# Kernel optimization log

Measured on AMD Instinct MI355X. Metric: run time of the kernel, lower is better.

Reference implementation:

```python
import jax, jax.numpy as jnp
import numpy as np

T, B = 1024, 256
OBS, ACT, GOAL = 64, 8, 16
NH, NH2 = 64, 64
H = NH + NH2  # 128 LSTM hidden


def _lin_init(k, out_d, in_d):
    bound = 1.0 / np.sqrt(in_d)
    k1, k2 = jax.random.split(k)
    w = jax.random.uniform(k1, (out_d, in_d), minval=-bound, maxval=bound, dtype=jnp.float32)
    b = jax.random.uniform(k2, (out_d,), minval=-bound, maxval=bound, dtype=jnp.float32)
    return w, b


def setup_inputs() -> dict:
    key = jax.random.key(0)
    ks = jax.random.split(key, 18)
    inp = {
        'observations': jax.random.normal(ks[0], (T, B, OBS), dtype=jnp.float32),
        'lps': jax.random.normal(ks[1], (T, B, 1), dtype=jnp.float32),
        'goal_eps': jax.random.normal(ks[2], (T, B, GOAL), dtype=jnp.float32),
        'action_eps': jax.random.normal(ks[3], (T, B, ACT), dtype=jnp.float32),
        'h0': jnp.zeros((2, B, H), jnp.float32),
        'c0': jnp.zeros((2, B, H), jnp.float32),
    }
    # LSTM (2 layers), torch layout: w_ih [4H, in], w_hh [4H, H]
    inp['w_ih0'], inp['b_ih0'] = _lin_init(ks[4], 4 * H, OBS + 1)
    inp['w_hh0'], inp['b_hh0'] = _lin_init(ks[5], 4 * H, H)
    inp['w_ih1'], inp['b_ih1'] = _lin_init(ks[6], 4 * H, H)
    inp['w_hh1'], inp['b_hh1'] = _lin_init(ks[7], 4 * H, H)
    # goal_decoder: MLP(NH, 2*GOAL), hidden = max(64, 32) = 64
    inp['gd_w1'], inp['gd_b1'] = _lin_init(ks[8], 64, NH)
    inp['gd_w2'], inp['gd_b2'] = _lin_init(ks[9], 2 * GOAL, 64)
    # action_decoder: MLP(GOAL+OBS=80, 2*ACT), hidden = 80
    inp['ad_w1'], inp['ad_b1'] = _lin_init(ks[10], GOAL + OBS, GOAL + OBS)
    inp['ad_w2'], inp['ad_b2'] = _lin_init(ks[11], 2 * ACT, GOAL + OBS)
    # value_decoder: MLP(80, 1), hidden = 80
    inp['vd_w1'], inp['vd_b1'] = _lin_init(ks[12], GOAL + OBS, GOAL + OBS)
    inp['vd_w2'], inp['vd_b2'] = _lin_init(ks[13], 1, GOAL + OBS)
    # lp_decoder: MLP(H+OBS=192, 1), hidden = 192
    inp['lpd_w1'], inp['lpd_b1'] = _lin_init(ks[14], H + OBS, H + OBS)
    inp['lpd_w2'], inp['lpd_b2'] = _lin_init(ks[15], 1, H + OBS)
    return inp


def _lstm_layer(x, h, c, wi, wh, bi, bh):
    def step(carry, xt):
        h, c = carry
        g = xt @ wi.T + h @ wh.T + (bi + bh)
        i, f, gg, o = jnp.split(g, 4, axis=-1)  # torch gate order: i, f, g, o
        i, f, o = jax.nn.sigmoid(i), jax.nn.sigmoid(f), jax.nn.sigmoid(o)
        c = f * c + i * jnp.tanh(gg)
        h = o * jnp.tanh(c)
        return (h, c), h
    _, hs = jax.lax.scan(step, (h, c), x)
    return hs  # [T, B, H]


def _mlp(x, w1, b1, w2, b2):
    return jax.nn.relu(x @ w1.T + b1) @ w2.T + b2


def _diag_logprob(x, mu, var):
    # log N(x; mu, diag(var))
    d = x.shape[-1]
    LOG_2PI = jnp.float32(np.log(2.0 * np.pi))
    return -0.5 * (jnp.sum((x - mu) ** 2 / var + jnp.log(var), axis=-1) + d * LOG_2PI)


def reference(observations, lps, goal_eps, action_eps, h0, c0,
              w_ih0, b_ih0, w_hh0, b_hh0, w_ih1, b_ih1, w_hh1, b_hh1,
              gd_w1, gd_b1, gd_w2, gd_b2, ad_w1, ad_b1, ad_w2, ad_b2,
              vd_w1, vd_b1, vd_w2, vd_b2, lpd_w1, lpd_b1, lpd_w2, lpd_b2):
    x = jnp.concatenate([observations, lps], axis=2)  # [T, B, OBS+1]
    h1 = _lstm_layer(x, h0[0], c0[0], w_ih0, w_hh0, b_ih0, b_hh0)
    latents_full = _lstm_layer(h1, h0[1], c0[1], w_ih1, w_hh1, b_ih1, b_hh1)  # [T,B,H]
    full_lat_obs = jnp.concatenate([latents_full, observations], axis=2)
    latents = latents_full[:, :, :NH]

    gm, gs = jnp.split(_mlp(latents, gd_w1, gd_b1, gd_w2, gd_b2), 2, axis=2)
    gm = 100.0 * jnp.tanh(gm * 0.001)
    gs = jnp.tanh(gs)
    gvar = gs ** 2 + 0.001
    goals = jax.lax.stop_gradient(gm + jnp.sqrt(gvar) * goal_eps)  # .sample() is non-diff
    log_prob_goals = _diag_logprob(goals, gm, gvar)

    goal_obs = jnp.concatenate([goals, observations], axis=2)
    am, asd = jnp.split(_mlp(goal_obs, ad_w1, ad_b1, ad_w2, ad_b2), 2, axis=2)
    avar = asd ** 2 + 0.001
    actions = jax.lax.stop_gradient(am + jnp.sqrt(avar) * action_eps)
    log_prob_actions = _diag_logprob(actions, am, avar)

    values = _mlp(goal_obs, vd_w1, vd_b1, vd_w2, vd_b2)
    lp_values = _mlp(full_lat_obs, lpd_w1, lpd_b1, lpd_w2, lpd_b2)
    return (actions, log_prob_actions, goals, log_prob_goals, values, lp_values)
```

## Files before the change

### kernel.cpp

```cpp
#include <hip/hip_runtime.h>
#include <hip/hip_bf16.h>
#include <math.h>

#define TT 1024
#define BB 256
#define LOG2PI 1.8378770664093453f

typedef short short8 __attribute__((ext_vector_type(8)));
typedef float f32x4  __attribute__((ext_vector_type(4)));

__device__ __forceinline__ float sigmoid_f(float x) {
    return 1.f / (1.f + __expf(-x));
}
__device__ __forceinline__ float tanh_f(float x) {
    return 1.f - 2.f / (__expf(2.f*x) + 1.f);
}
__device__ __forceinline__ unsigned short f2bf(float x) {
    unsigned int u = __float_as_uint(x);
    unsigned int r = (u + 0x7FFFu + ((u >> 16) & 1u)) >> 16;
    return (unsigned short)r;
}

#define MF(acc, a, bfr) acc = __builtin_amdgcn_mfma_f32_16x16x32_bf16((a), (bfr), (acc), 0, 0, 0)

__global__ __launch_bounds__(256) void cvt_bf16_kernel(
    const float* __restrict__ in, unsigned short* __restrict__ out)
{
    const int i = blockIdx.x*256 + threadIdx.x;
    const float4 a = ((const float4*)in)[2*i];
    const float4 b = ((const float4*)in)[2*i + 1];
    short8 v;
    v[0]=(short)f2bf(a.x); v[1]=(short)f2bf(a.y);
    v[2]=(short)f2bf(a.z); v[3]=(short)f2bf(a.w);
    v[4]=(short)f2bf(b.x); v[5]=(short)f2bf(b.y);
    v[6]=(short)f2bf(b.z); v[7]=(short)f2bf(b.w);
    ((short8*)out)[i] = v;
}

__global__ __launch_bounds__(256) void init_state_kernel(
    const float* __restrict__ h0, const float* __restrict__ c0,
    float* __restrict__ h_state, float* __restrict__ c_state)
{
    const int idx = blockIdx.x*256 + threadIdx.x;
    h_state[idx] = h0[idx];
    c_state[idx] = c0[idx];
}

__global__ __launch_bounds__(512, 2) void lstm0_kernel(
    const unsigned short* __restrict__ xb,
    const float* __restrict__ lps,
    const float* __restrict__ wi0,
    const float* __restrict__ wh0,
    const float* __restrict__ bi0, const float* __restrict__ bh0,
    float* __restrict__ h_state, float* __restrict__ c_state,
    unsigned short* __restrict__ h1_all,
    int steps)
{
    const int tid  = threadIdx.x;
    const int wave = tid >> 6;
    const int lane = tid & 63;
    const int b    = blockIdx.x;
    const int col  = lane & 15;
    const int kg   = lane >> 4;
    const int m    = wave*16 + col;

    __shared__ __align__(16) unsigned short s1_bf[2][128];

    short8 whf[4][4];
    short8 wxf[4][2];
    f32x4 wc64, bias4;
    #pragma unroll
    for (int tn = 0; tn < 4; ++tn) {
        const int j = tn*128 + m;
        #pragma unroll
        for (int ks = 0; ks < 4; ++ks) {
            const float* s = wh0 + (size_t)j*128 + ks*32 + kg*8;
            short8 v;
            #pragma unroll
            for (int i = 0; i < 8; ++i) v[i] = (short)f2bf(s[i]);
            whf[tn][ks] = v;
        }
        #pragma unroll
        for (int ks = 0; ks < 2; ++ks) {
            const float* s = wi0 + (size_t)j*65 + ks*32 + kg*8;
            short8 v;
            #pragma unroll
            for (int i = 0; i < 8; ++i) v[i] = (short)f2bf(s[i]);
            wxf[tn][ks] = v;
        }
        wc64[tn]  = wi0[(size_t)j*65 + 64];
        bias4[tn] = bi0[j] + bh0[j];
    }

    float c1 = 0.f, s1l = 0.f;
    if (kg == 0) {
        s1l = h_state[b*128 + m];
        c1  = c_state[b*128 + m];
        s1_bf[0][m] = f2bf(s1l);
    }
    const unsigned short* xp = xb + (size_t)b*64 + kg*8;
    const float* lpp = lps + b;
    short8 xA0 = *(const short8*)(xp);
    short8 xA1 = *(const short8*)(xp + 32);
    float  lpA = *lpp;
    xp  += (size_t)BB*64;
    lpp += BB;
    unsigned short* h1p = h1_all + (size_t)b*128 + m;

    asm volatile("s_waitcnt lgkmcnt(0)" ::: "memory");
    __builtin_amdgcn_s_barrier();
    __builtin_amdgcn_sched_barrier(0);

    #define STEP0(T_, RB, WB)                                                   \
    {                                                                           \
        short8 af0 = *(const short8*)&s1_bf[RB][0*32 + kg*8];                   \
        short8 af1 = *(const short8*)&s1_bf[RB][1*32 + kg*8];                   \
        short8 af2 = *(const short8*)&s1_bf[RB][2*32 + kg*8];                   \
        short8 af3 = *(const short8*)&s1_bf[RB][3*32 + kg*8];                   \
        short8 xu0 = xA0, xu1 = xA1;  float lpu = lpA;       \
        if ((T_) + 1 < steps) {                                                 \
            xA0 = *(const short8*)(xp);                                         \
            xA1 = *(const short8*)(xp + 32);                                    \
            lpA = *lpp;                                                         \
        }                                                                       \
        xp += (size_t)BB*64;  lpp += BB;                                        \
        f32x4 a0 = {0.f,0.f,0.f,0.f}, a1 = a0, a2 = a0, a3 = a0;                \
        MF(a0, af0, whf[0][0]); MF(a1, af0, whf[1][0]);                         \
        MF(a2, af0, whf[2][0]); MF(a3, af0, whf[3][0]);                         \
        MF(a0, af1, whf[0][1]); MF(a1, af1, whf[1][1]);                         \
        MF(a2, af1, whf[2][1]); MF(a3, af1, whf[3][1]);                         \
        MF(a0, af2, whf[0][2]); MF(a1, af2, whf[1][2]);                         \
        MF(a2, af2, whf[2][2]); MF(a3, af2, whf[3][2]);                         \
        MF(a0, af3, whf[0][3]); MF(a1, af3, whf[1][3]);                         \
        MF(a2, af3, whf[2][3]); MF(a3, af3, whf[3][3]);                         \
        MF(a0, xu0, wxf[0][0]); MF(a1, xu0, wxf[1][0]);                         \
        MF(a2, xu0, wxf[2][0]); MF(a3, xu0, wxf[3][0]);                         \
        MF(a0, xu1, wxf[0][1]); MF(a1, xu1, wxf[1][1]);                         \
        MF(a2, xu1, wxf[2][1]); MF(a3, xu1, wxf[3][1]);                         \
        if (kg == 0) {                                                          \
            float gi = a0[0] + bias4[0] + wc64[0]*lpu;                          \
            float gf = a1[0] + bias4[1] + wc64[1]*lpu;                          \
            float gg = a2[0] + bias4[2] + wc64[2]*lpu;                          \
            float go = a3[0] + bias4[3] + wc64[3]*lpu;                          \
            float iv = sigmoid_f(gi);                                           \
            float fv = sigmoid_f(gf);                                           \
            float gv = tanh_f(gg);                                              \
            float ov = sigmoid_f(go);                                           \
            c1 = fmaf(fv, c1, iv*gv);                                           \
            float hv = ov * tanh_f(c1);                                         \
            s1l = hv;                                                           \
            unsigned short hb = f2bf(hv);                                       \
            s1_bf[WB][m] = hb;                                                  \
            *h1p = hb;                                                          \
        }                                                                       \
        h1p += (size_t)BB*128;                                                  \
        asm volatile("s_waitcnt lgkmcnt(0)" ::: "memory");                      \
        __builtin_amdgcn_s_barrier();                                           \
        __builtin_amdgcn_sched_barrier(0);                                      \
    }

    for (int t = 0; t < steps; t += 2) {
        STEP0(t,     0, 1);
        STEP0(t + 1, 1, 0);
    }
    #undef STEP0

    if (kg == 0) {
        h_state[b*128 + m] = s1l;
        c_state[b*128 + m] = c1;
    }
}

__global__ __launch_bounds__(512, 2) void lstm1_kernel(
    const unsigned short* __restrict__ h1_all,
    const float* __restrict__ wi1, const float* __restrict__ wh1,
    const float* __restrict__ bi1, const float* __restrict__ bh1,
    float* __restrict__ h_state, float* __restrict__ c_state,
    float* __restrict__ h2_all,
    int steps)
{
    const int tid  = threadIdx.x;
    const int wave = tid >> 6;
    const int lane = tid & 63;
    const int b    = blockIdx.x;
    const int col  = lane & 15;
    const int kg   = lane >> 4;
    const int m    = wave*16 + col;

    __shared__ __align__(16) unsigned short s2_bf[2][128];

    short8 wif[4][4], whf[4][4];
    f32x4 bias4;
    #pragma unroll
    for (int tn = 0; tn < 4; ++tn) {
        const int j = tn*128 + m;
        #pragma unroll
        for (int ks = 0; ks < 4; ++ks) {
            const int ko = ks*32 + kg*8;
            const float* sa = wi1 + (size_t)j*128 + ko;
            const float* sb = wh1 + (size_t)j*128 + ko;
            short8 va, vb;
            #pragma unroll
            for (int i = 0; i < 8; ++i) {
                va[i] = (short)f2bf(sa[i]);
                vb[i] = (short)f2bf(sb[i]);
            }
            wif[tn][ks] = va;  whf[tn][ks] = vb;
        }
        bias4[tn] = bi1[j] + bh1[j];
    }

    float c2 = 0.f, s2l = 0.f;
    if (kg == 0) {
        s2l = h_state[b*128 + m];
        c2  = c_state[b*128 + m];
        s2_bf[0][m] = f2bf(s2l);
    }
    const unsigned short* sp = h1_all + (size_t)b*128 + kg*8;
    short8 sA0 = *(const short8*)(sp);
    short8 sA1 = *(const short8*)(sp + 32);
    short8 sA2 = *(const short8*)(sp + 64);
    short8 sA3 = *(const short8*)(sp + 96);
    sp += (size_t)BB*128;
    float* h2p = h2_all + (size_t)b*128 + m;

    asm volatile("s_waitcnt lgkmcnt(0)" ::: "memory");
    __builtin_amdgcn_s_barrier();
    __builtin_amdgcn_sched_barrier(0);

    #define STEP1(T_, RB, WB)                                                   \
    {                                                                           \
        short8 xu0 = sA0, xu1 = sA1, xu2 = sA2, xu3 = sA3;         \
        if ((T_) + 1 < steps) {                                                 \
            sA0 = *(const short8*)(sp);                                         \
            sA1 = *(const short8*)(sp + 32);                                    \
            sA2 = *(const short8*)(sp + 64);                                    \
            sA3 = *(const short8*)(sp + 96);                                    \
        }                                                                       \
        sp += (size_t)BB*128;                                                   \
        short8 af0 = *(const short8*)&s2_bf[RB][0*32 + kg*8];                   \
        short8 af1 = *(const short8*)&s2_bf[RB][1*32 + kg*8];                   \
        short8 af2 = *(const short8*)&s2_bf[RB][2*32 + kg*8];                   \
        short8 af3 = *(const short8*)&s2_bf[RB][3*32 + kg*8];                   \
        f32x4 b0 = {0.f,0.f,0.f,0.f}, b1 = b0, b2 = b0, b3 = b0;                \
        MF(b0, xu0, wif[0][0]); MF(b1, xu0, wif[1][0]);                         \
        MF(b2, xu0, wif[2][0]); MF(b3, xu0, wif[3][0]);                         \
        MF(b0, xu1, wif[0][1]); MF(b1, xu1, wif[1][1]);                         \
        MF(b2, xu1, wif[2][1]); MF(b3, xu1, wif[3][1]);                         \
        MF(b0, xu2, wif[0][2]); MF(b1, xu2, wif[1][2]);                         \
        MF(b2, xu2, wif[2][2]); MF(b3, xu2, wif[3][2]);                         \
        MF(b0, xu3, wif[0][3]); MF(b1, xu3, wif[1][3]);                         \
        MF(b2, xu3, wif[2][3]); MF(b3, xu3, wif[3][3]);                         \
        MF(b0, af0, whf[0][0]); MF(b1, af0, whf[1][0]);                         \
        MF(b2, af0, whf[2][0]); MF(b3, af0, whf[3][0]);                         \
        MF(b0, af1, whf[0][1]); MF(b1, af1, whf[1][1]);                         \
        MF(b2, af1, whf[2][1]); MF(b3, af1, whf[3][1]);                         \
        MF(b0, af2, whf[0][2]); MF(b1, af2, whf[1][2]);                         \
        MF(b2, af2, whf[2][2]); MF(b3, af2, whf[3][2]);                         \
        MF(b0, af3, whf[0][3]); MF(b1, af3, whf[1][3]);                         \
        MF(b2, af3, whf[2][3]); MF(b3, af3, whf[3][3]);                         \
        if (kg == 0) {                                                          \
            float iv = sigmoid_f(b0[0] + bias4[0]);                             \
            float fv = sigmoid_f(b1[0] + bias4[1]);                             \
            float gv = tanh_f   (b2[0] + bias4[2]);                             \
            float ov = sigmoid_f(b3[0] + bias4[3]);                             \
            c2 = fmaf(fv, c2, iv*gv);                                           \
            float hv = ov * tanh_f(c2);                                         \
            s2l = hv;                                                           \
            s2_bf[WB][m] = f2bf(hv);                                            \
            *h2p = hv;                                                          \
        }                                                                       \
        h2p += (size_t)BB*128;                                                  \
        asm volatile("s_waitcnt lgkmcnt(0)" ::: "memory");                      \
        __builtin_amdgcn_s_barrier();                                           \
        __builtin_amdgcn_sched_barrier(0);                                      \
    }

    for (int t = 0; t < steps; t += 2) {
        STEP1(t,     0, 1);
        STEP1(t + 1, 1, 0);
    }
    #undef STEP1

    if (kg == 0) {
        h_state[b*128 + m] = s2l;
        c_state[b*128 + m] = c2;
    }
}

__global__ __launch_bounds__(256) void dec_goal_kernel(
    const float* __restrict__ h2,
    const float* __restrict__ geps,
    const float* __restrict__ w1, const float* __restrict__ b1,
    const float* __restrict__ w2, const float* __restrict__ b2,
    float* __restrict__ out_goals, float* __restrict__ out_lpg)
{
    __shared__ float W1[64*64];
    __shared__ float W2[32*64];
    __shared__ float B1[64];
    __shared__ float B2[32];
    const int tid = threadIdx.x;
    for (int e = tid; e < 64*64; e += 256) W1[e] = w1[e];
    for (int e = tid; e < 32*64; e += 256) W2[e] = w2[e];
    if (tid < 64) B1[tid] = b1[tid];
    if (tid < 32) B2[tid] = b2[tid];
    __syncthreads();

    const size_t row = (size_t)blockIdx.x*256 + tid;
    const float* xr = h2 + row*128;

    float hid[64];
    #pragma unroll
    for (int jj = 0; jj < 64; ++jj) hid[jj] = B1[jj];
    for (int k = 0; k < 64; k += 4) {
        float4 xv = *(const float4*)(xr + k);
        #pragma unroll
        for (int jj = 0; jj < 64; ++jj) {
            float s = hid[jj];
            s = fmaf(W1[jj*64 + k],     xv.x, s);
            s = fmaf(W1[jj*64 + k + 1], xv.y, s);
            s = fmaf(W1[jj*64 + k + 2], xv.z, s);
            s = fmaf(W1[jj*64 + k + 3], xv.w, s);
            hid[jj] = s;
        }
    }
    #pragma unroll
    for (int jj = 0; jj < 64; ++jj) hid[jj] = fmaxf(hid[jj], 0.f);

    float gm[16];
    #pragma unroll
    for (int jj = 0; jj < 16; ++jj) {
        float s = B2[jj];
        #pragma unroll
        for (int k = 0; k < 64; ++k) s = fmaf(W2[jj*64 + k], hid[k], s);
        gm[jj] = 100.f * tanh_f(0.001f * s);
    }
    float ge[16];
    #pragma unroll
    for (int d = 0; d < 16; d += 4) {
        float4 v = *(const float4*)(geps + row*16 + d);
        ge[d]=v.x; ge[d+1]=v.y; ge[d+2]=v.z; ge[d+3]=v.w;
    }
    float lsum = 0.f;
    float goalv[16];
    #pragma unroll
    for (int jj = 0; jj < 16; ++jj) {
        float s = B2[16 + jj];
        #pragma unroll
        for (int k = 0; k < 64; ++k) s = fmaf(W2[(16+jj)*64 + k], hid[k], s);
        float gs   = tanh_f(s);
        float gvar = fmaf(gs, gs, 0.001f);
        float goal = fmaf(sqrtf(gvar), ge[jj], gm[jj]);
        goalv[jj] = goal;
        float dd = goal - gm[jj];
        lsum += dd*dd/gvar + __logf(gvar);
    }
    #pragma unroll
    for (int d = 0; d < 16; d += 4) {
        float4 v = make_float4(goalv[d], goalv[d+1], goalv[d+2], goalv[d+3]);
        *(float4*)(out_goals + row*16 + d) = v;
    }
    out_lpg[row] = -0.5f*(lsum + 16.f*LOG2PI);
}

__global__ __launch_bounds__(256) void dec_av_kernel(
    const float* __restrict__ goals,
    const float* __restrict__ obs,
    const float* __restrict__ aeps,
    const float* __restrict__ aw1, const float* __restrict__ ab1,
    const float* __restrict__ aw2, const float* __restrict__ ab2,
    const float* __restrict__ vw1, const float* __restrict__ vb1,
    const float* __restrict__ vw2, const float* __restrict__ vb2,
    float* __restrict__ out_actions, float* __restrict__ out_lpa,
    float* __restrict__ out_values)
{
    __shared__ float AW1[80*80];
    __shared__ float VW1[80*80];
    __shared__ float AW2[16*80];
    __shared__ float VW2[80];
    __shared__ float AB1[80];
    __shared__ float VB1[80];
    __shared__ float AB2[16];
    const int tid = threadIdx.x;
    for (int e = tid; e < 80*80; e += 256) { AW1[e] = aw1[e]; VW1[e] = vw1[e]; }
    for (int e = tid; e < 16*80; e += 256) AW2[e] = aw2[e];
    if (tid < 80) { VW2[tid] = vw2[tid]; AB1[tid] = ab1[tid]; VB1[tid] = vb1[tid]; }
    if (tid < 16) AB2[tid] = ab2[tid];
    __syncthreads();

    const size_t row = (size_t)blockIdx.x*256 + tid;

    float hid[80];
    #pragma unroll
    for (int jj = 0; jj < 80; ++jj) hid[jj] = AB1[jj];
    for (int k = 0; k < 80; k += 4) {
        float4 xv;
        if (k < 16) xv = *(const float4*)(goals + row*16 + k);
        else        xv = *(const float4*)(obs + row*64 + (k - 16));
        #pragma unroll
        for (int jj = 0; jj < 80; ++jj) {
            float s = hid[jj];
            s = fmaf(AW1[jj*80 + k],     xv.x, s);
            s = fmaf(AW1[jj*80 + k + 1], xv.y, s);
            s = fmaf(AW1[jj*80 + k + 2], xv.z, s);
            s = fmaf(AW1[jj*80 + k + 3], xv.w, s);
            hid[jj] = s;
        }
    }
    #pragma unroll
    for (int jj = 0; jj < 80; ++jj) hid[jj] = fmaxf(hid[jj], 0.f);

    float am[8], asd[8];
    #pragma unroll
    for (int jj = 0; jj < 8; ++jj) {
        float s = AB2[jj];
        #pragma unroll
        for (int k = 0; k < 80; ++k) s = fmaf(AW2[jj*80 + k], hid[k], s);
        am[jj] = s;
    }
    #pragma unroll
    for (int jj = 0; jj < 8; ++jj) {
        float s = AB2[8 + jj];
        #pragma unroll
        for (int k = 0; k < 80; ++k) s = fmaf(AW2[(8+jj)*80 + k], hid[k], s);
        asd[jj] = s;
    }

    float ae[8];
    #pragma unroll
    for (int d = 0; d < 8; d += 4) {
        float4 v = *(const float4*)(aeps + row*8 + d);
        ae[d]=v.x; ae[d+1]=v.y; ae[d+2]=v.z; ae[d+3]=v.w;
    }
    float lsum = 0.f;
    float actv[8];
    #pragma unroll
    for (int d = 0; d < 8; ++d) {
        float avar = fmaf(asd[d], asd[d], 0.001f);
        float act  = fmaf(sqrtf(avar), ae[d], am[d]);
        actv[d] = act;
        float dd = act - am[d];
        lsum += dd*dd/avar + __logf(avar);
    }
    #pragma unroll
    for (int d = 0; d < 8; d += 4) {
        float4 v = make_float4(actv[d], actv[d+1], actv[d+2], actv[d+3]);
        *(float4*)(out_actions + row*8 + d) = v;
    }
    out_lpa[row] = -0.5f*(lsum + 8.f*LOG2PI);

    float vh[80];
    #pragma unroll
    for (int jj = 0; jj < 80; ++jj) vh[jj] = VB1[jj];
    for (int k = 0; k < 80; k += 4) {
        float4 xv;
        if (k < 16) xv = *(const float4*)(goals + row*16 + k);
        else        xv = *(const float4*)(obs + row*64 + (k - 16));
        #pragma unroll
        for (int jj = 0; jj < 80; ++jj) {
            float s = vh[jj];
            s = fmaf(VW1[jj*80 + k],     xv.x, s);
            s = fmaf(VW1[jj*80 + k + 1], xv.y, s);
            s = fmaf(VW1[jj*80 + k + 2], xv.z, s);
            s = fmaf(VW1[jj*80 + k + 3], xv.w, s);
            vh[jj] = s;
        }
    }
    float v = vb2[0];
    #pragma unroll
    for (int jj = 0; jj < 80; ++jj) v = fmaf(VW2[jj], fmaxf(vh[jj], 0.f), v);
    out_values[row] = v;
}

__global__ __launch_bounds__(256) void dec_lpv_kernel(
    const float* __restrict__ h2,
    const float* __restrict__ obs,
    const float* __restrict__ w1, const float* __restrict__ b1,
    const float* __restrict__ w2, const float* __restrict__ b2,
    float* __restrict__ out_lpv)
{
    __shared__ __align__(16) float W1s[64*192];
    __shared__ float B1[192];
    __shared__ float W2[192];
    const int tid = threadIdx.x;
    const int l = tid & 3;
    const size_t item = (size_t)blockIdx.x*64 + (tid >> 2);
    if (tid < 192) { B1[tid] = b1[tid]; W2[tid] = w2[tid]; }

    float x[48];
    #pragma unroll
    for (int q = 0; q < 12; ++q) {
        int gk = l*48 + q*4;
        float4 v;
        if (gk < 128) v = *(const float4*)(h2 + item*128 + gk);
        else          v = *(const float4*)(obs + item*64 + (gk - 128));
        x[q*4]=v.x; x[q*4+1]=v.y; x[q*4+2]=v.z; x[q*4+3]=v.w;
    }

    float acc = 0.f;
    for (int j0 = 0; j0 < 192; j0 += 64) {
        __syncthreads();
        for (int e = tid; e < 64*48; e += 256) {
            int rr = e / 48, q = e - rr*48;
            *(float4*)&W1s[rr*192 + q*4] =
                *(const float4*)&w1[(size_t)(j0 + rr)*192 + q*4];
        }
        __syncthreads();
        for (int jj = 0; jj < 64; ++jj) {
            const float* wr = W1s + jj*192 + l*48;
            float p = 0.f;
            #pragma unroll
            for (int q = 0; q < 12; ++q) {
                float4 wv = *(const float4*)(wr + q*4);
                p = fmaf(wv.x, x[q*4],     p);
                p = fmaf(wv.y, x[q*4 + 1], p);
                p = fmaf(wv.z, x[q*4 + 2], p);
                p = fmaf(wv.w, x[q*4 + 3], p);
            }
            p += __shfl_xor(p, 1);
            p += __shfl_xor(p, 2);
            float h = fmaxf(p + B1[j0 + jj], 0.f);
            acc = fmaf(W2[j0 + jj], h, acc);
        }
    }
    if (l == 0) out_lpv[item] = acc + b2[0];
}

extern "C" void kernel_launch(void* const* d_in, const int* in_sizes, int n_in,
                              void* d_out, int out_size, void* d_ws, size_t ws_size,
                              hipStream_t stream)
{
    (void)in_sizes; (void)n_in; (void)out_size;

    const float* obs    = (const float*)d_in[0];
    const float* lps    = (const float*)d_in[1];
    const float* geps   = (const float*)d_in[2];
    const float* aeps   = (const float*)d_in[3];
    const float* h0     = (const float*)d_in[4];
    const float* c0     = (const float*)d_in[5];
    const float* w_ih0  = (const float*)d_in[6];
    const float* b_ih0  = (const float*)d_in[7];
    const float* w_hh0  = (const float*)d_in[8];
    const float* b_hh0  = (const float*)d_in[9];
    const float* w_ih1  = (const float*)d_in[10];
    const float* b_ih1  = (const float*)d_in[11];
    const float* w_hh1  = (const float*)d_in[12];
    const float* b_hh1  = (const float*)d_in[13];
    const float* gd_w1  = (const float*)d_in[14];
    const float* gd_b1  = (const float*)d_in[15];
    const float* gd_w2  = (const float*)d_in[16];
    const float* gd_b2  = (const float*)d_in[17];
    const float* ad_w1  = (const float*)d_in[18];
    const float* ad_b1  = (const float*)d_in[19];
    const float* ad_w2  = (const float*)d_in[20];
    const float* ad_b2  = (const float*)d_in[21];
    const float* vd_w1  = (const float*)d_in[22];
    const float* vd_b1  = (const float*)d_in[23];
    const float* vd_w2  = (const float*)d_in[24];
    const float* vd_b2  = (const float*)d_in[25];
    const float* lpd_w1 = (const float*)d_in[26];
    const float* lpd_b1 = (const float*)d_in[27];
    const float* lpd_w2 = (const float*)d_in[28];
    const float* lpd_b2 = (const float*)d_in[29];

    float* out         = (float*)d_out;
    float* out_actions = out;
    float* out_lpa     = out + 2097152;
    float* out_goals   = out + 2359296;
    float* out_lpg     = out + 6553600;
    float* out_values  = out + 6815744;
    float* out_lpv     = out + 7077888;

    const size_t XB_ELEMS    = (size_t)TT * BB * 64;
    const size_t STATE_ELEMS = 2ull * BB * 128;
    int C = 0;
    for (int c = TT; c >= 8; c >>= 1) {
        size_t need = XB_ELEMS*2
                    + (size_t)c * BB * 128 * 2
                    + (size_t)c * BB * 128 * 4
                    + 2 * STATE_ELEMS * 4;
        if (need <= ws_size) { C = c; break; }
    }
    if (C == 0) return;
    const int nchunks = TT / C;

    unsigned short* xb  = (unsigned short*)d_ws;
    unsigned short* h1c = xb + XB_ELEMS;
    float* h2c     = (float*)(h1c + (size_t)C * BB * 128);
    float* h_state = h2c + (size_t)C * BB * 128;
    float* c_state = h_state + STATE_ELEMS;

    const dim3 blk(256);

    cvt_bf16_kernel<<<dim3((int)(XB_ELEMS/8/256)), blk, 0, stream>>>(obs, xb);
    init_state_kernel<<<dim3((int)(STATE_ELEMS/256)), blk, 0, stream>>>(
        h0, c0, h_state, c_state);

    for (int ch = 0; ch < nchunks; ++ch) {
        const size_t crow0 = (size_t)ch * C * BB;
        const int rows = C * BB;

        lstm0_kernel<<<dim3(BB), dim3(512), 0, stream>>>(
            xb + crow0*64, lps + crow0, w_ih0, w_hh0, b_ih0, b_hh0,
            h_state, c_state, h1c, C);

        lstm1_kernel<<<dim3(BB), dim3(512), 0, stream>>>(
            h1c, w_ih1, w_hh1, b_ih1, b_hh1,
            h_state + BB*128, c_state + BB*128, h2c, C);

        dec_goal_kernel<<<dim3(rows/256), blk, 0, stream>>>(
            h2c, geps + crow0*16, gd_w1, gd_b1, gd_w2, gd_b2,
            out_goals + crow0*16, out_lpg + crow0);

        dec_av_kernel<<<dim3(rows/256), blk, 0, stream>>>(
            out_goals + crow0*16, obs + crow0*64, aeps + crow0*8,
            ad_w1, ad_b1, ad_w2, ad_b2, vd_w1, vd_b1, vd_w2, vd_b2,
            out_actions + crow0*8, out_lpa + crow0, out_values + crow0);

        dec_lpv_kernel<<<dim3(rows/64), blk, 0, stream>>>(
            h2c, obs + crow0*64, lpd_w1, lpd_b1, lpd_w2, lpd_b2,
            out_lpv + crow0);
    }
}
```

Before: 2.377 ms.

## Precompute next step's input-projection MFMAs before the barrier in LSTM kernels

Moves the input-to-hidden MFMA work for step t+1 to the end of step t, after the gate update and before the barrier, so the critical path after each barrier holds only the recurrent h@Wh MFMAs. Global loads of x/h1 now run two steps ahead. Launch bounds drop from 2 to 1 blocks per CU, giving the compiler more registers for the live accumulators. This cuts serial latency per timestep but may lower occupancy.

Result: slower. 2.669 ms (+12.3%).

```diff
diff --git a/kernel.cpp b/kernel.cpp
--- a/kernel.cpp
+++ b/kernel.cpp
@@ -46,7 +46,7 @@
     c_state[idx] = c0[idx];
 }
 
-__global__ __launch_bounds__(512, 2) void lstm0_kernel(
+__global__ __launch_bounds__(512, 1) void lstm0_kernel(
     const unsigned short* __restrict__ xb,
     const float* __restrict__ lps,
     const float* __restrict__ wi0,
@@ -102,9 +102,21 @@
     const float* lpp = lps + b;
     short8 xA0 = *(const short8*)(xp);
     short8 xA1 = *(const short8*)(xp + 32);
-    float  lpA = *lpp;
-    xp  += (size_t)BB*64;
+    xp += (size_t)BB*64;
+    float lpA = *lpp;
     lpp += BB;
+
+    f32x4 a0 = {0.f,0.f,0.f,0.f}, a1 = a0, a2 = a0, a3 = a0;
+    MF(a0, xA0, wxf[0][0]); MF(a1, xA0, wxf[1][0]);
+    MF(a2, xA0, wxf[2][0]); MF(a3, xA0, wxf[3][0]);
+    MF(a0, xA1, wxf[0][1]); MF(a1, xA1, wxf[1][1]);
+    MF(a2, xA1, wxf[2][1]); MF(a3, xA1, wxf[3][1]);
+    if (steps > 1) {
+        xA0 = *(const short8*)(xp);
+        xA1 = *(const short8*)(xp + 32);
+    }
+    xp += (size_t)BB*64;
+
     unsigned short* h1p = h1_all + (size_t)b*128 + m;
 
     asm volatile("s_waitcnt lgkmcnt(0)" ::: "memory");
@@ -117,14 +129,6 @@
         short8 af1 = *(const short8*)&s1_bf[RB][1*32 + kg*8];                   \
         short8 af2 = *(const short8*)&s1_bf[RB][2*32 + kg*8];                   \
         short8 af3 = *(const short8*)&s1_bf[RB][3*32 + kg*8];                   \
-        short8 xu0 = xA0, xu1 = xA1;  float lpu = lpA;       \
-        if ((T_) + 1 < steps) {                                                 \
-            xA0 = *(const short8*)(xp);                                         \
-            xA1 = *(const short8*)(xp + 32);                                    \
-            lpA = *lpp;                                                         \
-        }                                                                       \
-        xp += (size_t)BB*64;  lpp += BB;                                        \
-        f32x4 a0 = {0.f,0.f,0.f,0.f}, a1 = a0, a2 = a0, a3 = a0;                \
         MF(a0, af0, whf[0][0]); MF(a1, af0, whf[1][0]);                         \
         MF(a2, af0, whf[2][0]); MF(a3, af0, whf[3][0]);                         \
         MF(a0, af1, whf[0][1]); MF(a1, af1, whf[1][1]);                         \
@@ -133,15 +137,11 @@
         MF(a2, af2, whf[2][2]); MF(a3, af2, whf[3][2]);                         \
         MF(a0, af3, whf[0][3]); MF(a1, af3, whf[1][3]);                         \
         MF(a2, af3, whf[2][3]); MF(a3, af3, whf[3][3]);                         \
-        MF(a0, xu0, wxf[0][0]); MF(a1, xu0, wxf[1][0]);                         \
-        MF(a2, xu0, wxf[2][0]); MF(a3, xu0, wxf[3][0]);                         \
-        MF(a0, xu1, wxf[0][1]); MF(a1, xu1, wxf[1][1]);                         \
-        MF(a2, xu1, wxf[2][1]); MF(a3, xu1, wxf[3][1]);                         \
         if (kg == 0) {                                                          \
-            float gi = a0[0] + bias4[0] + wc64[0]*lpu;                          \
-            float gf = a1[0] + bias4[1] + wc64[1]*lpu;                          \
-            float gg = a2[0] + bias4[2] + wc64[2]*lpu;                          \
-            float go = a3[0] + bias4[3] + wc64[3]*lpu;                          \
+            float gi = a0[0] + bias4[0] + wc64[0]*lpA;                          \
+            float gf = a1[0] + bias4[1] + wc64[1]*lpA;                          \
+            float gg = a2[0] + bias4[2] + wc64[2]*lpA;                          \
+            float go = a3[0] + bias4[3] + wc64[3]*lpA;                          \
             float iv = sigmoid_f(gi);                                           \
             float fv = sigmoid_f(gf);                                           \
             float gv = tanh_f(gg);                                              \
@@ -154,6 +154,18 @@
             *h1p = hb;                                                          \
         }                                                                       \
         h1p += (size_t)BB*128;                                                  \
+        if ((T_) + 1 < steps) lpA = *lpp;     \
+        lpp += BB;                                                              \
+        a0 = (f32x4){0.f,0.f,0.f,0.f}; a1 = a0; a2 = a0; a3 = a0;               \
+        MF(a0, xA0, wxf[0][0]); MF(a1, xA0, wxf[1][0]);                         \
+        MF(a2, xA0, wxf[2][0]); MF(a3, xA0, wxf[3][0]);                         \
+        MF(a0, xA1, wxf[0][1]); MF(a1, xA1, wxf[1][1]);                         \
+        MF(a2, xA1, wxf[2][1]); MF(a3, xA1, wxf[3][1]);                         \
+        if ((T_) + 2 < steps) {                 \
+            xA0 = *(const short8*)(xp);                                         \
+            xA1 = *(const short8*)(xp + 32);                                    \
+        }                                                                       \
+        xp += (size_t)BB*64;                                                    \
         asm volatile("s_waitcnt lgkmcnt(0)" ::: "memory");                      \
         __builtin_amdgcn_s_barrier();                                           \
         __builtin_amdgcn_sched_barrier(0);                                      \
@@ -171,7 +183,7 @@
     }
 }
 
-__global__ __launch_bounds__(512, 2) void lstm1_kernel(
+__global__ __launch_bounds__(512, 1) void lstm1_kernel(
     const unsigned short* __restrict__ h1_all,
     const float* __restrict__ wi1, const float* __restrict__ wh1,
     const float* __restrict__ bi1, const float* __restrict__ bh1,
@@ -222,6 +234,24 @@
     short8 sA2 = *(const short8*)(sp + 64);
     short8 sA3 = *(const short8*)(sp + 96);
     sp += (size_t)BB*128;
+
+    f32x4 b0 = {0.f,0.f,0.f,0.f}, b1 = b0, b2 = b0, b3 = b0;
+    MF(b0, sA0, wif[0][0]); MF(b1, sA0, wif[1][0]);
+    MF(b2, sA0, wif[2][0]); MF(b3, sA0, wif[3][0]);
+    MF(b0, sA1, wif[0][1]); MF(b1, sA1, wif[1][1]);
+    MF(b2, sA1, wif[2][1]); MF(b3, sA1, wif[3][1]);
+    MF(b0, sA2, wif[0][2]); MF(b1, sA2, wif[1][2]);
+    MF(b2, sA2, wif[2][2]); MF(b3, sA2, wif[3][2]);
+    MF(b0, sA3, wif[0][3]); MF(b1, sA3, wif[1][3]);
+    MF(b2, sA3, wif[2][3]); MF(b3, sA3, wif[3][3]);
+    if (steps > 1) {
+        sA0 = *(const short8*)(sp);
+        sA1 = *(const short8*)(sp + 32);
+        sA2 = *(const short8*)(sp + 64);
+        sA3 = *(const short8*)(sp + 96);
+    }
+    sp += (size_t)BB*128;
+
     float* h2p = h2_all + (size_t)b*128 + m;
 
     asm volatile("s_waitcnt lgkmcnt(0)" ::: "memory");
@@ -230,27 +260,10 @@
 
     #define STEP1(T_, RB, WB)                                                   \
     {                                                                           \
-        short8 xu0 = sA0, xu1 = sA1, xu2 = sA2, xu3 = sA3;         \
-        if ((T_) + 1 < steps) {                                                 \
-            sA0 = *(const short8*)(sp);                                         \
-            sA1 = *(const short8*)(sp + 32);                                    \
-            sA2 = *(const short8*)(sp + 64);                                    \
-            sA3 = *(const short8*)(sp + 96);                                    \
-        }                                                                       \
-        sp += (size_t)BB*128;                                                   \
         short8 af0 = *(const short8*)&s2_bf[RB][0*32 + kg*8];                   \
         short8 af1 = *(const short8*)&s2_bf[RB][1*32 + kg*8];                   \
         short8 af2 = *(const short8*)&s2_bf[RB][2*32 + kg*8];                   \
         short8 af3 = *(const short8*)&s2_bf[RB][3*32 + kg*8];                   \
-        f32x4 b0 = {0.f,0.f,0.f,0.f}, b1 = b0, b2 = b0, b3 = b0;                \
-        MF(b0, xu0, wif[0][0]); MF(b1, xu0, wif[1][0]);                         \
-        MF(b2, xu0, wif[2][0]); MF(b3, xu0, wif[3][0]);                         \
-        MF(b0, xu1, wif[0][1]); MF(b1, xu1, wif[1][1]);                         \
-        MF(b2, xu1, wif[2][1]); MF(b3, xu1, wif[3][1]);                         \
-        MF(b0, xu2, wif[0][2]); MF(b1, xu2, wif[1][2]);                         \
-        MF(b2, xu2, wif[2][2]); MF(b3, xu2, wif[3][2]);                         \
-        MF(b0, xu3, wif[0][3]); MF(b1, xu3, wif[1][3]);                         \
-        MF(b2, xu3, wif[2][3]); MF(b3, xu3, wif[3][3]);                         \
         MF(b0, af0, whf[0][0]); MF(b1, af0, whf[1][0]);                         \
         MF(b2, af0, whf[2][0]); MF(b3, af0, whf[3][0]);                         \
         MF(b0, af1, whf[0][1]); MF(b1, af1, whf[1][1]);                         \
@@ -271,6 +284,22 @@
             *h2p = hv;                                                          \
         }                                                                       \
         h2p += (size_t)BB*128;                                                  \
+        b0 = (f32x4){0.f,0.f,0.f,0.f}; b1 = b0; b2 = b0; b3 = b0;               \
+        MF(b0, sA0, wif[0][0]); MF(b1, sA0, wif[1][0]);                         \
+        MF(b2, sA0, wif[2][0]); MF(b3, sA0, wif[3][0]);                         \
+        MF(b0, sA1, wif[0][1]); MF(b1, sA1, wif[1][1]);                         \
+        MF(b2, sA1, wif[2][1]); MF(b3, sA1, wif[3][1]);                         \
+        MF(b0, sA2, wif[0][2]); MF(b1, sA2, wif[1][2]);                         \
+        MF(b2, sA2, wif[2][2]); MF(b3, sA2, wif[3][2]);                         \
+        MF(b0, sA3, wif[0][3]); MF(b1, sA3, wif[1][3]);                         \
+        MF(b2, sA3, wif[2][3]); MF(b3, sA3, wif[3][3]);                         \
+        if ((T_) + 2 < steps) {                 \
+            sA0 = *(const short8*)(sp);                                         \
+            sA1 = *(const short8*)(sp + 32);                                    \
+            sA2 = *(const short8*)(sp + 64);                                    \
+            sA3 = *(const short8*)(sp + 96);                                    \
+        }                                                                       \
+        sp += (size_t)BB*128;                                                   \
         asm volatile("s_waitcnt lgkmcnt(0)" ::: "memory");                      \
         __builtin_amdgcn_s_barrier();                                           \
         __builtin_amdgcn_sched_barrier(0);                                      \
```

## Fuse both LSTM layers into one producer-consumer kernel with progress flags

Applied to the files above, without the earlier changes.

Replaces the two sequential LSTM kernels with one launch of 2*BB blocks. The first half runs layer 0 and publishes per-batch progress counters with release stores. The second half runs layer 1, spin-waiting on those counters every 8 steps, so the two recurrences overlap in time instead of running back to back. The gain depends on all 512 blocks being co-resident, since producers and consumers spin on each other. It also adds polling and acquire/release overhead plus a small reset kernel per chunk.

New measurement: 6.515 ms. 2.74x slower.

```diff
diff --git a/kernel.cpp b/kernel.cpp
--- a/kernel.cpp
+++ b/kernel.cpp
@@ -46,245 +46,283 @@
     c_state[idx] = c0[idx];
 }
 
-__global__ __launch_bounds__(512, 2) void lstm0_kernel(
+__global__ __launch_bounds__(256) void reset_prog_kernel(unsigned* prog)
+{
+    prog[threadIdx.x] = 0u;
+}
+
+__global__ __launch_bounds__(512, 2) void lstm_pc_kernel(
     const unsigned short* __restrict__ xb,
     const float* __restrict__ lps,
     const float* __restrict__ wi0,
     const float* __restrict__ wh0,
     const float* __restrict__ bi0, const float* __restrict__ bh0,
-    float* __restrict__ h_state, float* __restrict__ c_state,
-    unsigned short* __restrict__ h1_all,
-    int steps)
-{
-    const int tid  = threadIdx.x;
-    const int wave = tid >> 6;
-    const int lane = tid & 63;
-    const int b    = blockIdx.x;
-    const int col  = lane & 15;
-    const int kg   = lane >> 4;
-    const int m    = wave*16 + col;
-
-    __shared__ __align__(16) unsigned short s1_bf[2][128];
-
-    short8 whf[4][4];
-    short8 wxf[4][2];
-    f32x4 wc64, bias4;
-    #pragma unroll
-    for (int tn = 0; tn < 4; ++tn) {
-        const int j = tn*128 + m;
-        #pragma unroll
-        for (int ks = 0; ks < 4; ++ks) {
-            const float* s = wh0 + (size_t)j*128 + ks*32 + kg*8;
-            short8 v;
-            #pragma unroll
-            for (int i = 0; i < 8; ++i) v[i] = (short)f2bf(s[i]);
-            whf[tn][ks] = v;
-        }
-        #pragma unroll
-        for (int ks = 0; ks < 2; ++ks) {
-            const float* s = wi0 + (size_t)j*65 + ks*32 + kg*8;
-            short8 v;
-            #pragma unroll
-            for (int i = 0; i < 8; ++i) v[i] = (short)f2bf(s[i]);
-            wxf[tn][ks] = v;
-        }
-        wc64[tn]  = wi0[(size_t)j*65 + 64];
-        bias4[tn] = bi0[j] + bh0[j];
-    }
-
-    float c1 = 0.f, s1l = 0.f;
-    if (kg == 0) {
-        s1l = h_state[b*128 + m];
-        c1  = c_state[b*128 + m];
-        s1_bf[0][m] = f2bf(s1l);
-    }
-    const unsigned short* xp = xb + (size_t)b*64 + kg*8;
-    const float* lpp = lps + b;
-    short8 xA0 = *(const short8*)(xp);
-    short8 xA1 = *(const short8*)(xp + 32);
-    float  lpA = *lpp;
-    xp  += (size_t)BB*64;
-    lpp += BB;
-    unsigned short* h1p = h1_all + (size_t)b*128 + m;
-
-    asm volatile("s_waitcnt lgkmcnt(0)" ::: "memory");
-    __builtin_amdgcn_s_barrier();
-    __builtin_amdgcn_sched_barrier(0);
-
-    #define STEP0(T_, RB, WB)                                                   \
-    {                                                                           \
-        short8 af0 = *(const short8*)&s1_bf[RB][0*32 + kg*8];                   \
-        short8 af1 = *(const short8*)&s1_bf[RB][1*32 + kg*8];                   \
-        short8 af2 = *(const short8*)&s1_bf[RB][2*32 + kg*8];                   \
-        short8 af3 = *(const short8*)&s1_bf[RB][3*32 + kg*8];                   \
-        short8 xu0 = xA0, xu1 = xA1;  float lpu = lpA;       \
-        if ((T_) + 1 < steps) {                                                 \
-            xA0 = *(const short8*)(xp);                                         \
-            xA1 = *(const short8*)(xp + 32);                                    \
-            lpA = *lpp;                                                         \
-        }                                                                       \
-        xp += (size_t)BB*64;  lpp += BB;                                        \
-        f32x4 a0 = {0.f,0.f,0.f,0.f}, a1 = a0, a2 = a0, a3 = a0;                \
-        MF(a0, af0, whf[0][0]); MF(a1, af0, whf[1][0]);                         \
-        MF(a2, af0, whf[2][0]); MF(a3, af0, whf[3][0]);                         \
-        MF(a0, af1, whf[0][1]); MF(a1, af1, whf[1][1]);                         \
-        MF(a2, af1, whf[2][1]); MF(a3, af1, whf[3][1]);                         \
-        MF(a0, af2, whf[0][2]); MF(a1, af2, whf[1][2]);                         \
-        MF(a2, af2, whf[2][2]); MF(a3, af2, whf[3][2]);                         \
-        MF(a0, af3, whf[0][3]); MF(a1, af3, whf[1][3]);                         \
-        MF(a2, af3, whf[2][3]); MF(a3, af3, whf[3][3]);                         \
-        MF(a0, xu0, wxf[0][0]); MF(a1, xu0, wxf[1][0]);                         \
-        MF(a2, xu0, wxf[2][0]); MF(a3, xu0, wxf[3][0]);                         \
-        MF(a0, xu1, wxf[0][1]); MF(a1, xu1, wxf[1][1]);                         \
-        MF(a2, xu1, wxf[2][1]); MF(a3, xu1, wxf[3][1]);                         \
-        if (kg == 0) {                                                          \
-            float gi = a0[0] + bias4[0] + wc64[0]*lpu;                          \
-            float gf = a1[0] + bias4[1] + wc64[1]*lpu;                          \
-            float gg = a2[0] + bias4[2] + wc64[2]*lpu;                          \
-            float go = a3[0] + bias4[3] + wc64[3]*lpu;                          \
-            float iv = sigmoid_f(gi);                                           \
-            float fv = sigmoid_f(gf);                                           \
-            float gv = tanh_f(gg);                                              \
-            float ov = sigmoid_f(go);                                           \
-            c1 = fmaf(fv, c1, iv*gv);                                           \
-            float hv = ov * tanh_f(c1);                                         \
-            s1l = hv;                                                           \
-            unsigned short hb = f2bf(hv);                                       \
-            s1_bf[WB][m] = hb;                                                  \
-            *h1p = hb;                                                          \
-        }                                                                       \
-        h1p += (size_t)BB*128;                                                  \
-        asm volatile("s_waitcnt lgkmcnt(0)" ::: "memory");                      \
-        __builtin_amdgcn_s_barrier();                                           \
-        __builtin_amdgcn_sched_barrier(0);                                      \
-    }
-
-    for (int t = 0; t < steps; t += 2) {
-        STEP0(t,     0, 1);
-        STEP0(t + 1, 1, 0);
-    }
-    #undef STEP0
-
-    if (kg == 0) {
-        h_state[b*128 + m] = s1l;
-        c_state[b*128 + m] = c1;
-    }
-}
-
-__global__ __launch_bounds__(512, 2) void lstm1_kernel(
-    const unsigned short* __restrict__ h1_all,
+    unsigned short* h1_all,
     const float* __restrict__ wi1, const float* __restrict__ wh1,
     const float* __restrict__ bi1, const float* __restrict__ bh1,
     float* __restrict__ h_state, float* __restrict__ c_state,
     float* __restrict__ h2_all,
+    unsigned* prog,
     int steps)
 {
     const int tid  = threadIdx.x;
     const int wave = tid >> 6;
     const int lane = tid & 63;
-    const int b    = blockIdx.x;
     const int col  = lane & 15;
     const int kg   = lane >> 4;
     const int m    = wave*16 + col;
 
-    __shared__ __align__(16) unsigned short s2_bf[2][128];
-
-    short8 wif[4][4], whf[4][4];
-    f32x4 bias4;
-    #pragma unroll
-    for (int tn = 0; tn < 4; ++tn) {
-        const int j = tn*128 + m;
-        #pragma unroll
-        for (int ks = 0; ks < 4; ++ks) {
-            const int ko = ks*32 + kg*8;
-            const float* sa = wi1 + (size_t)j*128 + ko;
-            const float* sb = wh1 + (size_t)j*128 + ko;
-            short8 va, vb;
+    __shared__ __align__(16) unsigned short st_bf[2][128];
+
+    if (blockIdx.x < BB) {
+        const int b = blockIdx.x;
+        unsigned* pg = prog + b;
+
+        short8 whf[4][4];
+        short8 wxf[4][2];
+        f32x4 wc64, bias4;
+        #pragma unroll
+        for (int tn = 0; tn < 4; ++tn) {
+            const int j = tn*128 + m;
             #pragma unroll
-            for (int i = 0; i < 8; ++i) {
-                va[i] = (short)f2bf(sa[i]);
-                vb[i] = (short)f2bf(sb[i]);
+            for (int ks = 0; ks < 4; ++ks) {
+                const float* s = wh0 + (size_t)j*128 + ks*32 + kg*8;
+                short8 v;
+                #pragma unroll
+                for (int i = 0; i < 8; ++i) v[i] = (short)f2bf(s[i]);
+                whf[tn][ks] = v;
             }
-            wif[tn][ks] = va;  whf[tn][ks] = vb;
-        }
-        bias4[tn] = bi1[j] + bh1[j];
-    }
-
-    float c2 = 0.f, s2l = 0.f;
-    if (kg == 0) {
-        s2l = h_state[b*128 + m];
-        c2  = c_state[b*128 + m];
-        s2_bf[0][m] = f2bf(s2l);
-    }
-    const unsigned short* sp = h1_all + (size_t)b*128 + kg*8;
-    short8 sA0 = *(const short8*)(sp);
-    short8 sA1 = *(const short8*)(sp + 32);
-    short8 sA2 = *(const short8*)(sp + 64);
-    short8 sA3 = *(const short8*)(sp + 96);
-    sp += (size_t)BB*128;
-    float* h2p = h2_all + (size_t)b*128 + m;
-
-    asm volatile("s_waitcnt lgkmcnt(0)" ::: "memory");
-    __builtin_amdgcn_s_barrier();
-    __builtin_amdgcn_sched_barrier(0);
-
-    #define STEP1(T_, RB, WB)                                                   \
-    {                                                                           \
-        short8 xu0 = sA0, xu1 = sA1, xu2 = sA2, xu3 = sA3;         \
-        if ((T_) + 1 < steps) {                                                 \
-            sA0 = *(const short8*)(sp);                                         \
-            sA1 = *(const short8*)(sp + 32);                                    \
-            sA2 = *(const short8*)(sp + 64);                                    \
-            sA3 = *(const short8*)(sp + 96);                                    \
-        }                                                                       \
-        sp += (size_t)BB*128;                                                   \
-        short8 af0 = *(const short8*)&s2_bf[RB][0*32 + kg*8];                   \
-        short8 af1 = *(const short8*)&s2_bf[RB][1*32 + kg*8];                   \
-        short8 af2 = *(const short8*)&s2_bf[RB][2*32 + kg*8];                   \
-        short8 af3 = *(const short8*)&s2_bf[RB][3*32 + kg*8];                   \
-        f32x4 b0 = {0.f,0.f,0.f,0.f}, b1 = b0, b2 = b0, b3 = b0;                \
-        MF(b0, xu0, wif[0][0]); MF(b1, xu0, wif[1][0]);                         \
-        MF(b2, xu0, wif[2][0]); MF(b3, xu0, wif[3][0]);                         \
-        MF(b0, xu1, wif[0][1]); MF(b1, xu1, wif[1][1]);                         \
-        MF(b2, xu1, wif[2][1]); MF(b3, xu1, wif[3][1]);                         \
-        MF(b0, xu2, wif[0][2]); MF(b1, xu2, wif[1][2]);                         \
-        MF(b2, xu2, wif[2][2]); MF(b3, xu2, wif[3][2]);                         \
-        MF(b0, xu3, wif[0][3]); MF(b1, xu3, wif[1][3]);                         \
-        MF(b2, xu3, wif[2][3]); MF(b3, xu3, wif[3][3]);                         \
-        MF(b0, af0, whf[0][0]); MF(b1, af0, whf[1][0]);                         \
-        MF(b2, af0, whf[2][0]); MF(b3, af0, whf[3][0]);                         \
-        MF(b0, af1, whf[0][1]); MF(b1, af1, whf[1][1]);                         \
-        MF(b2, af1, whf[2][1]); MF(b3, af1, whf[3][1]);                         \
-        MF(b0, af2, whf[0][2]); MF(b1, af2, whf[1][2]);                         \
-        MF(b2, af2, whf[2][2]); MF(b3, af2, whf[3][2]);                         \
-        MF(b0, af3, whf[0][3]); MF(b1, af3, whf[1][3]);                         \
-        MF(b2, af3, whf[2][3]); MF(b3, af3, whf[3][3]);                         \
-        if (kg == 0) {                                                          \
-            float iv = sigmoid_f(b0[0] + bias4[0]);                             \
-            float fv = sigmoid_f(b1[0] + bias4[1]);                             \
-            float gv = tanh_f   (b2[0] + bias4[2]);                             \
-            float ov = sigmoid_f(b3[0] + bias4[3]);                             \
-            c2 = fmaf(fv, c2, iv*gv);                                           \
-            float hv = ov * tanh_f(c2);                                         \
-            s2l = hv;                                                           \
-            s2_bf[WB][m] = f2bf(hv);                                            \
-            *h2p = hv;                                                          \
-        }                                                                       \
-        h2p += (size_t)BB*128;                                                  \
-        asm volatile("s_waitcnt lgkmcnt(0)" ::: "memory");                      \
-        __builtin_amdgcn_s_barrier();                                           \
-        __builtin_amdgcn_sched_barrier(0);                                      \
-    }
-
-    for (int t = 0; t < steps; t += 2) {
-        STEP1(t,     0, 1);
-        STEP1(t + 1, 1, 0);
-    }
-    #undef STEP1
-
-    if (kg == 0) {
-        h_state[b*128 + m] = s2l;
-        c_state[b*128 + m] = c2;
+            #pragma unroll
+            for (int ks = 0; ks < 2; ++ks) {
+                const float* s = wi0 + (size_t)j*65 + ks*32 + kg*8;
+                short8 v;
+                #pragma unroll
+                for (int i = 0; i < 8; ++i) v[i] = (short)f2bf(s[i]);
+                wxf[tn][ks] = v;
+            }
+            wc64[tn]  = wi0[(size_t)j*65 + 64];
+            bias4[tn] = bi0[j] + bh0[j];
+        }
+
+        float c1 = 0.f, s1l = 0.f;
+        if (kg == 0) {
+            s1l = h_state[b*128 + m];
+            c1  = c_state[b*128 + m];
+            st_bf[0][m] = f2bf(s1l);
+        }
+        const unsigned short* xp = xb + (size_t)b*64 + kg*8;
+        const float* lpp = lps + b;
+        short8 xA0 = *(const short8*)(xp);
+        short8 xA1 = *(const short8*)(xp + 32);
+        float  lpA = *lpp;
+        xp  += (size_t)BB*64;
+        lpp += BB;
+        unsigned short* h1p = h1_all + (size_t)b*128 + m;
+
+        asm volatile("s_waitcnt lgkmcnt(0)" ::: "memory");
+        __builtin_amdgcn_s_barrier();
+        __builtin_amdgcn_sched_barrier(0);
+
+        #define STEP0(T_, RB, WB)                                               \
+        {                                                                       \
+            short8 af0 = *(const short8*)&st_bf[RB][0*32 + kg*8];               \
+            short8 af1 = *(const short8*)&st_bf[RB][1*32 + kg*8];               \
+            short8 af2 = *(const short8*)&st_bf[RB][2*32 + kg*8];               \
+            short8 af3 = *(const short8*)&st_bf[RB][3*32 + kg*8];               \
+            f32x4 a0 = {0.f,0.f,0.f,0.f}, a1 = a0, a2 = a0, a3 = a0;            \
+            MF(a0, af0, whf[0][0]); MF(a1, af0, whf[1][0]);                     \
+            MF(a2, af0, whf[2][0]); MF(a3, af0, whf[3][0]);                     \
+            MF(a0, af1, whf[0][1]); MF(a1, af1, whf[1][1]);                     \
+            MF(a2, af1, whf[2][1]); MF(a3, af1, whf[3][1]);                     \
+            MF(a0, af2, whf[0][2]); MF(a1, af2, whf[1][2]);                     \
+            MF(a2, af2, whf[2][2]); MF(a3, af2, whf[3][2]);                     \
+            MF(a0, af3, whf[0][3]); MF(a1, af3, whf[1][3]);                     \
+            MF(a2, af3, whf[2][3]); MF(a3, af3, whf[3][3]);                     \
+            MF(a0, xA0, wxf[0][0]); MF(a1, xA0, wxf[1][0]);                     \
+            MF(a2, xA0, wxf[2][0]); MF(a3, xA0, wxf[3][0]);                     \
+            MF(a0, xA1, wxf[0][1]); MF(a1, xA1, wxf[1][1]);                     \
+            MF(a2, xA1, wxf[2][1]); MF(a3, xA1, wxf[3][1]);                     \
+            if ((T_) + 1 < steps) {                                             \
+                xA0 = *(const short8*)(xp);                                     \
+                xA1 = *(const short8*)(xp + 32);                                \
+            }                                                                   \
+            xp += (size_t)BB*64;                                                \
+            if (kg == 0) {                                                      \
+                float gi = a0[0] + bias4[0] + wc64[0]*lpA;                      \
+                float gf = a1[0] + bias4[1] + wc64[1]*lpA;                      \
+                float gg = a2[0] + bias4[2] + wc64[2]*lpA;                      \
+                float go = a3[0] + bias4[3] + wc64[3]*lpA;                      \
+                float iv = sigmoid_f(gi);                                       \
+                float fv = sigmoid_f(gf);                                       \
+                float gv = tanh_f(gg);                                          \
+                float ov = sigmoid_f(go);                                       \
+                c1 = fmaf(fv, c1, iv*gv);                                       \
+                float hv = ov * tanh_f(c1);                                     \
+                s1l = hv;                                                       \
+                unsigned short hb = f2bf(hv);                                   \
+                st_bf[WB][m] = hb;                                              \
+                *h1p = hb;                                                      \
+            }                                                                   \
+            h1p += (size_t)BB*128;                                              \
+            if ((T_) + 1 < steps) lpA = *lpp;                                   \
+            lpp += BB;                                                          \
+            asm volatile("s_waitcnt lgkmcnt(0)" ::: "memory");                  \
+            __builtin_amdgcn_s_barrier();                                       \
+            __builtin_amdgcn_sched_barrier(0);                                  \
+        }
+
+        for (int t = 0; t < steps; t += 8) {
+            STEP0(t,     0, 1);
+            STEP0(t + 1, 1, 0);
+            STEP0(t + 2, 0, 1);
+            STEP0(t + 3, 1, 0);
+            STEP0(t + 4, 0, 1);
+            STEP0(t + 5, 1, 0);
+            STEP0(t + 6, 0, 1);
+            STEP0(t + 7, 1, 0);
+            __threadfence();
+            __builtin_amdgcn_s_barrier();
+            if (tid == 0)
+                __hip_atomic_store(pg, (unsigned)(t + 8),
+                                   __ATOMIC_RELEASE, __HIP_MEMORY_SCOPE_AGENT);
+        }
+        #undef STEP0
+
+        if (kg == 0) {
+            h_state[b*128 + m] = s1l;
+            c_state[b*128 + m] = c1;
+        }
+    } else {
+        const int b = blockIdx.x - BB;
+        unsigned* pg = prog + b;
+
+        short8 wif[4][4], whf[4][4];
+        f32x4 bias4;
+        #pragma unroll
+        for (int tn = 0; tn < 4; ++tn) {
+            const int j = tn*128 + m;
+            #pragma unroll
+            for (int ks = 0; ks < 4; ++ks) {
+                const int ko = ks*32 + kg*8;
+                const float* sa = wi1 + (size_t)j*128 + ko;
+                const float* sb = wh1 + (size_t)j*128 + ko;
+                short8 va, vb;
+                #pragma unroll
+                for (int i = 0; i < 8; ++i) {
+                    va[i] = (short)f2bf(sa[i]);
+                    vb[i] = (short)f2bf(sb[i]);
+                }
+                wif[tn][ks] = va;  whf[tn][ks] = vb;
+            }
+            bias4[tn] = bi1[j] + bh1[j];
+        }
+
+        float c2 = 0.f, s2l = 0.f;
+        if (kg == 0) {
+            s2l = h_state[(BB + b)*128 + m];
+            c2  = c_state[(BB + b)*128 + m];
+            st_bf[0][m] = f2bf(s2l);
+        }
+
+        {
+            const unsigned tgt = (steps < 16) ? (unsigned)steps : 16u;
+            if (tid == 0) {
+                while (__hip_atomic_load(pg, __ATOMIC_RELAXED,
+                                         __HIP_MEMORY_SCOPE_AGENT) < tgt)
+                    __builtin_amdgcn_s_sleep(32);
+                (void)__hip_atomic_load(pg, __ATOMIC_ACQUIRE,
+                                        __HIP_MEMORY_SCOPE_AGENT);
+            }
+            __builtin_amdgcn_s_barrier();
+        }
+
+        const unsigned short* sp = h1_all + (size_t)b*128 + kg*8;
+        short8 sA0 = *(const short8*)(sp);
+        short8 sA1 = *(const short8*)(sp + 32);
+        short8 sA2 = *(const short8*)(sp + 64);
+        short8 sA3 = *(const short8*)(sp + 96);
+        sp += (size_t)BB*128;
+        float* h2p = h2_all + (size_t)b*128 + m;
+
+        asm volatile("s_waitcnt lgkmcnt(0)" ::: "memory");
+        __builtin_amdgcn_s_barrier();
+        __builtin_amdgcn_sched_barrier(0);
+
+        #define STEP1(T_, RB, WB)                                               \
+        {                                                                       \
+            short8 af0 = *(const short8*)&st_bf[RB][0*32 + kg*8];               \
+            short8 af1 = *(const short8*)&st_bf[RB][1*32 + kg*8];               \
+            short8 af2 = *(const short8*)&st_bf[RB][2*32 + kg*8];               \
+            short8 af3 = *(const short8*)&st_bf[RB][3*32 + kg*8];               \
+            f32x4 b0 = {0.f,0.f,0.f,0.f}, b1 = b0, b2 = b0, b3 = b0;            \
+            MF(b0, sA0, wif[0][0]); MF(b1, sA0, wif[1][0]);                     \
+            MF(b2, sA0, wif[2][0]); MF(b3, sA0, wif[3][0]);                     \
+            MF(b0, sA1, wif[0][1]); MF(b1, sA1, wif[1][1]);                     \
+            MF(b2, sA1, wif[2][1]); MF(b3, sA1, wif[3][1]);                     \
+            MF(b0, sA2, wif[0][2]); MF(b1, sA2, wif[1][2]);                     \
+            MF(b2, sA2, wif[2][2]); MF(b3, sA2, wif[3][2]);                     \
+            MF(b0, sA3, wif[0][3]); MF(b1, sA3, wif[1][3]);                     \
+            MF(b2, sA3, wif[2][3]); MF(b3, sA3, wif[3][3]);                     \
+            if ((T_) + 1 < steps) {                                             \
+                sA0 = *(const short8*)(sp);                                     \
+                sA1 = *(const short8*)(sp + 32);                                \
+                sA2 = *(const short8*)(sp + 64);                                \
+                sA3 = *(const short8*)(sp + 96);                                \
+            }                                                                   \
+            sp += (size_t)BB*128;                                               \
+            MF(b0, af0, whf[0][0]); MF(b1, af0, whf[1][0]);                     \
+            MF(b2, af0, whf[2][0]); MF(b3, af0, whf[3][0]);                     \
+            MF(b0, af1, whf[0][1]); MF(b1, af1, whf[1][1]);                     \
+            MF(b2, af1, whf[2][1]); MF(b3, af1, whf[3][1]);                     \
+            MF(b0, af2, whf[0][2]); MF(b1, af2, whf[1][2]);                     \
+            MF(b2, af2, whf[2][2]); MF(b3, af2, whf[3][2]);                     \
+            MF(b0, af3, whf[0][3]); MF(b1, af3, whf[1][3]);                     \
+            MF(b2, af3, whf[2][3]); MF(b3, af3, whf[3][3]);                     \
+            if (kg == 0) {                                                      \
+                float iv = sigmoid_f(b0[0] + bias4[0]);                         \
+                float fv = sigmoid_f(b1[0] + bias4[1]);                         \
+                float gv = tanh_f   (b2[0] + bias4[2]);                         \
+                float ov = sigmoid_f(b3[0] + bias4[3]);                         \
+                c2 = fmaf(fv, c2, iv*gv);                                       \
+                float hv = ov * tanh_f(c2);                                     \
+                s2l = hv;                                                       \
+                st_bf[WB][m] = f2bf(hv);                                        \
+                *h2p = hv;                                                      \
+            }                                                                   \
+            h2p += (size_t)BB*128;                                              \
+            asm volatile("s_waitcnt lgkmcnt(0)" ::: "memory");                  \
+            __builtin_amdgcn_s_barrier();                                       \
+            __builtin_amdgcn_sched_barrier(0);                                  \
+        }
+
+        for (int t = 0; t < steps; t += 8) {
+            if (t) {
+                const unsigned tgt = (t + 16 < steps) ? (unsigned)(t + 16)
+                                                      : (unsigned)steps;
+                if (tid == 0) {
+                    while (__hip_atomic_load(pg, __ATOMIC_RELAXED,
+                                             __HIP_MEMORY_SCOPE_AGENT) < tgt)
+                        __builtin_amdgcn_s_sleep(32);
+                    (void)__hip_atomic_load(pg, __ATOMIC_ACQUIRE,
+                                            __HIP_MEMORY_SCOPE_AGENT);
+                }
+                __builtin_amdgcn_s_barrier();
+            }
+            STEP1(t,     0, 1);
+            STEP1(t + 1, 1, 0);
+            STEP1(t + 2, 0, 1);
+            STEP1(t + 3, 1, 0);
+            STEP1(t + 4, 0, 1);
+            STEP1(t + 5, 1, 0);
+            STEP1(t + 6, 0, 1);
+            STEP1(t + 7, 1, 0);
+        }
+        #undef STEP1
+
+        if (kg == 0) {
+            h_state[(BB + b)*128 + m] = s2l;
+            c_state[(BB + b)*128 + m] = c2;
+        }
     }
 }
 
@@ -578,7 +616,8 @@
         size_t need = XB_ELEMS*2
                     + (size_t)c * BB * 128 * 2
                     + (size_t)c * BB * 128 * 4
-                    + 2 * STATE_ELEMS * 4;
+                    + 2 * STATE_ELEMS * 4
+                    + BB * 4;
         if (need <= ws_size) { C = c; break; }
     }
     if (C == 0) return;
@@ -589,6 +628,7 @@
     float* h2c     = (float*)(h1c + (size_t)C * BB * 128);
     float* h_state = h2c + (size_t)C * BB * 128;
     float* c_state = h_state + STATE_ELEMS;
+    unsigned* prog = (unsigned*)(c_state + STATE_ELEMS);
 
     const dim3 blk(256);
 
@@ -600,13 +640,14 @@
         const size_t crow0 = (size_t)ch * C * BB;
         const int rows = C * BB;
 
-        lstm0_kernel<<<dim3(BB), dim3(512), 0, stream>>>(
-            xb + crow0*64, lps + crow0, w_ih0, w_hh0, b_ih0, b_hh0,
-            h_state, c_state, h1c, C);
-
-        lstm1_kernel<<<dim3(BB), dim3(512), 0, stream>>>(
-            h1c, w_ih1, w_hh1, b_ih1, b_hh1,
-            h_state + BB*128, c_state + BB*128, h2c, C);
+        reset_prog_kernel<<<dim3(1), blk, 0, stream>>>(prog);
+
+        lstm_pc_kernel<<<dim3(2*BB), dim3(512), 0, stream>>>(
+            xb + crow0*64, lps + crow0,
+            w_ih0, w_hh0, b_ih0, b_hh0,
+            h1c,
+            w_ih1, w_hh1, b_ih1, b_hh1,
+            h_state, c_state, h2c, prog, C);
 
         dec_goal_kernel<<<dim3(rows/256), blk, 0, stream>>>(
             h2c, geps + crow0*16, gd_w1, gd_b1, gd_w2, gd_b2,
```
